# Kernel tuning notes

Measured on AMD Instinct MI355X. Metric: run time of the kernel, lower is better.

Reference implementation:

```python
import jax, jax.numpy as jnp
import numpy as np

HEADS = 16
DIM_HEAD = 64
SCALE = DIM_HEAD ** -0.5
NEG = -jnp.finfo(jnp.float32).max


def setup_inputs() -> dict:
    key = jax.random.key(0)
    ks = jax.random.split(key, 5)
    b, n, dim = 2, 2048, 1024
    inner = HEADS * DIM_HEAD
    s = dim ** -0.5  # keep pre-softmax logits well-scaled
    return {
        "x": jax.random.normal(ks[0], (b, n, dim), jnp.float32),
        "mask": jnp.ones((b, n), dtype=bool),
        "Wq": jax.random.normal(ks[1], (dim, inner), jnp.float32) * s,
        "Wk": jax.random.normal(ks[2], (dim, inner), jnp.float32) * s,
        "Wv": jax.random.normal(ks[3], (dim, inner), jnp.float32) * s,
        "Wo": jax.random.normal(ks[4], (inner, dim), jnp.float32) * s,
    }


def reference(x, mask, Wq, Wk, Wv, Wo):
    b, n, _ = x.shape
    # projections, split heads: b n (h d) -> b h n d
    def split(t):
        return t.reshape(b, n, HEADS, DIM_HEAD).transpose(0, 2, 1, 3)
    q = split(x @ Wq)
    k = split(x @ Wk)
    v = split(x @ Wv)
    dots = jnp.einsum("bhid,bhjd->bhij", q, k) * SCALE  # [b,h,n,n]
    # padding mask: b j -> b 1 1 j
    dots = jnp.where(mask[:, None, None, :], dots, NEG)
    # causal mask (strict upper triangle masked)
    causal = jnp.triu(jnp.ones((n, n), dtype=bool), k=1)
    dots = jnp.where(causal, NEG, dots)
    attn = jax.nn.softmax(dots, axis=-1)
    out = jnp.einsum("bhij,bhjd->bhid", attn, v)
    out = out.transpose(0, 2, 1, 3).reshape(b, n, HEADS * DIM_HEAD)
    return out @ Wo
```

## Files before the change

kernel.cpp:

```cpp
#include <hip/hip_runtime.h>
#include <hip/hip_bf16.h>

typedef __bf16 bf16x8 __attribute__((ext_vector_type(8)));
typedef float f32x4 __attribute__((ext_vector_type(4)));
typedef unsigned short u16;
typedef unsigned int u32;

#define MFMA16(A, B, C) __builtin_amdgcn_mfma_f32_16x16x32_bf16((A), (B), (C), 0, 0, 0)

#define BATCH 2
#define SEQ   2048
#define DIM   1024
#define NHEAD 16
#define DHEAD 64
#define MROWS 4096
#define Q_SCALE 0.18033688f

__device__ __forceinline__ u16 f2bf(float f) {
    unsigned int u = __float_as_uint(f);
    u += 0x7fff + ((u >> 16) & 1);
    return (u16)(u >> 16);
}

__device__ __forceinline__ u32 pk2bf(float a, float b) {
    __hip_bfloat162 c = __float22bfloat162_rn(float2{a, b});
    u32 r;
    __builtin_memcpy(&r, &c, 4);
    return r;
}

__device__ __forceinline__ void glds16(const u16* g, u16* l) {
    __builtin_amdgcn_global_load_lds(
        (const __attribute__((address_space(1))) u32*)g,
        (__attribute__((address_space(3))) u32*)l, 16, 0, 0);
}

__global__ __launch_bounds__(256) void cvt_x(const float* __restrict__ x,
                                             u16* __restrict__ xb) {
    int i = (blockIdx.x * 256 + threadIdx.x) * 8;
    float4 a = *(const float4*)(x + i);
    float4 b = *(const float4*)(x + i + 4);
    u16 o[8] = {f2bf(a.x), f2bf(a.y), f2bf(a.z), f2bf(a.w),
                f2bf(b.x), f2bf(b.y), f2bf(b.z), f2bf(b.w)};
    *(uint4*)(xb + i) = *(uint4*)o;
}

__global__ __launch_bounds__(256) void cvt_w_t(const float* __restrict__ wq,
                                               const float* __restrict__ wk,
                                               const float* __restrict__ wv,
                                               const float* __restrict__ wo,
                                               u16* __restrict__ wt) {
    __shared__ u16 tile[64][65];
    const float* W = (blockIdx.z == 0) ? wq : (blockIdx.z == 1) ? wk
                   : (blockIdx.z == 2) ? wv : wo;
    u16* out = wt + (size_t)blockIdx.z * DIM * DIM;
    int k0 = blockIdx.x * 64;
    int n0 = blockIdx.y * 64;
    int t = threadIdx.x;
    int c = t & 63, r4 = t >> 6;
#pragma unroll
    for (int i = 0; i < 16; i++) {
        int row = i * 4 + r4;
        tile[row][c] = f2bf(W[(size_t)(k0 + row) * DIM + n0 + c]);
    }
    __syncthreads();
#pragma unroll
    for (int i = 0; i < 16; i++) {
        int row = i * 4 + r4;
        out[(size_t)(n0 + row) * DIM + k0 + c] = tile[c][row];
    }
}

__global__ __launch_bounds__(256) void gemm_qkv(const u16* __restrict__ xb,
                                                const u16* __restrict__ wt,
                                                u16* __restrict__ qb,
                                                u16* __restrict__ kb,
                                                u16* __restrict__ vtb) {
    __shared__ __align__(16) u16 As[128 * 32];
    __shared__ __align__(16) u16 Bs[128 * 32];
    const int z = blockIdx.z;
    const u16* W = wt + (size_t)z * DIM * DIM;
    const int m0 = blockIdx.y * 128, n0 = blockIdx.x * 128;
    const int t = threadIdx.x, w = t >> 6, lane = t & 63;
    const int quad = lane >> 4, l16 = lane & 15;
    const int wm = (w >> 1) * 64, wn = (w & 1) * 64;
    const int srow = lane >> 2, skc = (lane & 3) * 8;

    f32x4 acc[4][4] = {};
    for (int k0 = 0; k0 < DIM; k0 += 32) {
        if (k0) __syncthreads();
#pragma unroll
        for (int j = 0; j < 2; j++) {
            int rb = w * 32 + j * 16;
            glds16(&xb[(size_t)(m0 + rb + srow) * DIM + k0 + skc], &As[rb * 32]);
            glds16(&W[(size_t)(n0 + rb + srow) * DIM + k0 + skc], &Bs[rb * 32]);
        }
        __syncthreads();

        bf16x8 af[4], bfr[4];
#pragma unroll
        for (int mt = 0; mt < 4; mt++)
            af[mt] = *(const bf16x8*)&As[(wm + mt * 16 + l16) * 32 + quad * 8];
#pragma unroll
        for (int nt = 0; nt < 4; nt++)
            bfr[nt] = *(const bf16x8*)&Bs[(wn + nt * 16 + l16) * 32 + quad * 8];
#pragma unroll
        for (int mt = 0; mt < 4; mt++)
#pragma unroll
            for (int nt = 0; nt < 4; nt++)
                acc[mt][nt] = MFMA16(af[mt], bfr[nt], acc[mt][nt]);
    }
    const float sc = (z == 0) ? Q_SCALE : 1.0f;
#pragma unroll
    for (int mt = 0; mt < 4; mt++)
#pragma unroll
        for (int nt = 0; nt < 4; nt++)
#pragma unroll
            for (int r = 0; r < 4; r++) {
                int gm = m0 + wm + mt * 16 + quad * 4 + r;
                int gc = n0 + wn + nt * 16 + l16;
                int bi = gm >> 11, si = gm & (SEQ - 1);
                int h = gc >> 6, d = gc & 63;
                u16 v = f2bf(acc[mt][nt][r] * sc);
                if (z == 0)
                    qb[(((size_t)bi * NHEAD + h) * SEQ + si) * DHEAD + d] = v;
                else if (z == 1)
                    kb[(((size_t)bi * NHEAD + h) * SEQ + si) * DHEAD + d] = v;
                else
                    vtb[(((size_t)bi * NHEAD + h) * DHEAD + d) * SEQ + si] = v;
            }
}

#define LPAD 72
__global__ __launch_bounds__(256) void attn(const u16* __restrict__ qg,
                                            const u16* __restrict__ kg,
                                            const u16* __restrict__ vtg,
                                            u16* __restrict__ og) {
    __shared__ __align__(16) u16 Ks[2][64 * LPAD];
    __shared__ __align__(16) u16 Vs[2][64 * LPAD];
    __shared__ __align__(16) u16 Ps[64 * LPAD];

    const int bh = blockIdx.y;
    const int t = threadIdx.x, w = t >> 6, lane = t & 63;
    const int quad = lane >> 4, l16 = lane & 15;
    const int srow = t >> 2, sc16 = (t & 3) * 16;
    const size_t qkrow = (size_t)bh * SEQ;
    const size_t vrow = (size_t)bh * DHEAD;
    const int bi = bh >> 4, h = bh & 15;

    uint4 pk0, pk1, pv0, pv1;
    auto prefetch = [&](int j0) {
        const u16* kp = &kg[(qkrow + j0 + srow) * DHEAD + sc16];
        pk0 = *(const uint4*)kp;
        pk1 = *(const uint4*)(kp + 8);
        const u16* vp = &vtg[(vrow + srow) * SEQ + j0 + sc16];
        pv0 = *(const uint4*)vp;
        pv1 = *(const uint4*)(vp + 8);
    };

    u16* prow = &Ps[(w * 16 + l16) * LPAD];

    for (int half = 0; half < 2; half++) {
        const int qt = half ? (31 - (int)blockIdx.x) : (int)blockIdx.x;
        const int q0 = qt * 64;
        const int last = qt;
        const int rowmin = q0 + w * 16;
        const int rowq = rowmin + l16;

        const u16* qp = qg + (qkrow + rowq) * DHEAD;
        bf16x8 aq0 = *(const bf16x8*)(qp + quad * 8);
        bf16x8 aq1 = *(const bf16x8*)(qp + 32 + quad * 8);

        f32x4 accO[4] = {};
        float l_part = 0.f;

        prefetch(0);
        __syncthreads();

        for (int jt = 0; jt <= last; jt++) {
            const int buf = jt & 1;
            u16* ksb = &Ks[buf][0];
            u16* vsb = &Vs[buf][0];
            *(uint4*)&ksb[srow * LPAD + sc16] = pk0;
            *(uint4*)&ksb[srow * LPAD + sc16 + 8] = pk1;
            *(uint4*)&vsb[srow * LPAD + sc16] = pv0;
            *(uint4*)&vsb[srow * LPAD + sc16 + 8] = pv1;
            __syncthreads();
            if (jt < last) prefetch((jt + 1) * 64);

            const int j0 = jt * 64;
            if (j0 > rowmin + 15) continue;
            const bool need_mask = (j0 + 63 > rowmin);

            f32x4 s[4];
#pragma unroll
            for (int nt = 0; nt < 4; nt++) {
                bf16x8 ak0 = *(const bf16x8*)&ksb[(nt * 16 + l16) * LPAD + quad * 8];
                bf16x8 ak1 = *(const bf16x8*)&ksb[(nt * 16 + l16) * LPAD + 32 + quad * 8];
                f32x4 a = {};
                a = MFMA16(ak0, aq0, a);
                a = MFMA16(ak1, aq1, a);
                s[nt] = a;
            }

#pragma unroll
            for (int nt = 0; nt < 4; nt++) {
                float p[4];
                if (need_mask) {
                    int kbase = j0 + nt * 16 + quad * 4;
#pragma unroll
                    for (int r = 0; r < 4; r++)
                        p[r] = (kbase + r > rowq) ? 0.f
                             : __builtin_amdgcn_exp2f(s[nt][r]);
                } else {
#pragma unroll
                    for (int r = 0; r < 4; r++)
                        p[r] = __builtin_amdgcn_exp2f(s[nt][r]);
                }
                l_part += (p[0] + p[1]) + (p[2] + p[3]);
                uint2 pkd = {pk2bf(p[0], p[1]), pk2bf(p[2], p[3])};
                *(uint2*)&prow[nt * 16 + quad * 4] = pkd;
            }

            bf16x8 bp0 = *(const bf16x8*)&prow[quad * 8];
            bf16x8 bp1 = *(const bf16x8*)&prow[32 + quad * 8];
#pragma unroll
            for (int mt = 0; mt < 4; mt++) {
                bf16x8 av0 = *(const bf16x8*)&vsb[(mt * 16 + l16) * LPAD + quad * 8];
                bf16x8 av1 = *(const bf16x8*)&vsb[(mt * 16 + l16) * LPAD + 32 + quad * 8];
                accO[mt] = MFMA16(av0, bp0, accO[mt]);
                accO[mt] = MFMA16(av1, bp1, accO[mt]);
            }
        }

        l_part += __shfl_xor(l_part, 16);
        l_part += __shfl_xor(l_part, 32);
        float rl = 1.0f / l_part;
        size_t obase = ((size_t)bi * SEQ + rowq) * DIM + h * DHEAD;
#pragma unroll
        for (int mt = 0; mt < 4; mt++) {
            uint2 pkd = {pk2bf(accO[mt][0] * rl, accO[mt][1] * rl),
                         pk2bf(accO[mt][2] * rl, accO[mt][3] * rl)};
            *(uint2*)&og[obase + mt * 16 + quad * 4] = pkd;
        }
    }
}

__global__ __launch_bounds__(256) void gemm_out(const u16* __restrict__ ob,
                                                const u16* __restrict__ wot,
                                                float* __restrict__ out) {
    __shared__ __align__(16) u16 As[64 * 32];
    __shared__ __align__(16) u16 Bs[128 * 32];
    const int m0 = blockIdx.y * 64, n0 = blockIdx.x * 128;
    const int t = threadIdx.x, w = t >> 6, lane = t & 63;
    const int quad = lane >> 4, l16 = lane & 15;
    const int wm = (w >> 1) * 32, wn = (w & 1) * 64;
    const int srow = lane >> 2, skc = (lane & 3) * 8;

    f32x4 acc[2][4] = {};
    for (int k0 = 0; k0 < DIM; k0 += 32) {
        if (k0) __syncthreads();
        glds16(&ob[(size_t)(m0 + w * 16 + srow) * DIM + k0 + skc], &As[w * 16 * 32]);
#pragma unroll
        for (int j = 0; j < 2; j++) {
            int rb = w * 32 + j * 16;
            glds16(&wot[(size_t)(n0 + rb + srow) * DIM + k0 + skc], &Bs[rb * 32]);
        }
        __syncthreads();

        bf16x8 af[2], bfr[4];
#pragma unroll
        for (int mt = 0; mt < 2; mt++)
            af[mt] = *(const bf16x8*)&As[(wm + mt * 16 + l16) * 32 + quad * 8];
#pragma unroll
        for (int nt = 0; nt < 4; nt++)
            bfr[nt] = *(const bf16x8*)&Bs[(wn + nt * 16 + l16) * 32 + quad * 8];
#pragma unroll
        for (int mt = 0; mt < 2; mt++)
#pragma unroll
            for (int nt = 0; nt < 4; nt++)
                acc[mt][nt] = MFMA16(af[mt], bfr[nt], acc[mt][nt]);
    }
#pragma unroll
    for (int mt = 0; mt < 2; mt++)
#pragma unroll
        for (int nt = 0; nt < 4; nt++)
#pragma unroll
            for (int r = 0; r < 4; r++) {
                int gm = m0 + wm + mt * 16 + quad * 4 + r;
                int gc = n0 + wn + nt * 16 + l16;
                out[(size_t)gm * DIM + gc] = acc[mt][nt][r];
            }
}

extern "C" void kernel_launch(void* const* d_in, const int* in_sizes, int n_in,
                              void* d_out, int out_size, void* d_ws, size_t ws_size,
                              hipStream_t stream) {
    const float* x  = (const float*)d_in[0];
    const float* wq = (const float*)d_in[2];
    const float* wk = (const float*)d_in[3];
    const float* wv = (const float*)d_in[4];
    const float* wo = (const float*)d_in[5];
    float* out = (float*)d_out;

    char* ws = (char*)d_ws;
    u16* xb  = (u16*)(ws);
    u16* wt  = (u16*)(ws + (8ull  << 20));
    u16* qb  = (u16*)(ws + (16ull << 20));
    u16* kb  = (u16*)(ws + (24ull << 20));
    u16* vtb = (u16*)(ws + (32ull << 20));
    u16* obf = (u16*)(ws + (40ull << 20));

    cvt_x<<<MROWS * DIM / (256 * 8), 256, 0, stream>>>(x, xb);
    cvt_w_t<<<dim3(16, 16, 4), 256, 0, stream>>>(wq, wk, wv, wo, wt);
    gemm_qkv<<<dim3(DIM / 128, MROWS / 128, 3), 256, 0, stream>>>(xb, wt, qb, kb, vtb);
    attn<<<dim3(16, BATCH * NHEAD), 256, 0, stream>>>(qb, kb, vtb, obf);
    gemm_out<<<dim3(DIM / 128, MROWS / 64), 256, 0, stream>>>(
        obf, wt + 3ull * DIM * DIM, out);
}
```

Measured before the change: 191.7 us.

## Rework attention kernel to 32x32 MFMA with key-split waves and async LDS staging

Replaces the attention inner loop's 16x16x32 MFMAs with 32x32x16 MFMAs. Each wave now owns 32 query rows and one 32-key half of each 64-key tile, and the two key halves are reduced through shared memory at the end. K/V tiles are staged with direct global-to-LDS loads (glds16) into XOR-swizzled unpadded buffers, issued before compute to overlap with the current tile. This aims to cut LDS fragment loads and register-staging overhead, at the cost of extra shared memory for the output reduction, an additional barrier, and waves idling on masked key halves.

```diff
diff --git a/kernel.cpp b/kernel.cpp
--- a/kernel.cpp
+++ b/kernel.cpp
@@ -3,10 +3,12 @@
 
 typedef __bf16 bf16x8 __attribute__((ext_vector_type(8)));
 typedef float f32x4 __attribute__((ext_vector_type(4)));
+typedef float f32x16 __attribute__((ext_vector_type(16)));
 typedef unsigned short u16;
 typedef unsigned int u32;
 
 #define MFMA16(A, B, C) __builtin_amdgcn_mfma_f32_16x16x32_bf16((A), (B), (C), 0, 0, 0)
+#define MFMA32(A, B, C) __builtin_amdgcn_mfma_f32_32x32x16_bf16((A), (B), (C), 0, 0, 0)
 
 #define BATCH 2
 #define SEQ   2048
@@ -136,112 +138,131 @@
                                             const u16* __restrict__ kg,
                                             const u16* __restrict__ vtg,
                                             u16* __restrict__ og) {
-    __shared__ __align__(16) u16 Ks[2][64 * LPAD];
-    __shared__ __align__(16) u16 Vs[2][64 * LPAD];
+    __shared__ __align__(16) u16 Ks[2][64 * 64];
+    __shared__ __align__(16) u16 Vs[2][64 * 64];
     __shared__ __align__(16) u16 Ps[64 * LPAD];
+    __shared__ __align__(16) float Os[4096];
+    __shared__ float Ls[64];
 
     const int bh = blockIdx.y;
     const int t = threadIdx.x, w = t >> 6, lane = t & 63;
-    const int quad = lane >> 4, l16 = lane & 15;
-    const int srow = t >> 2, sc16 = (t & 3) * 16;
-    const size_t qkrow = (size_t)bh * SEQ;
-    const size_t vrow = (size_t)bh * DHEAD;
-    const int bi = bh >> 4, h = bh & 15;
-
-    uint4 pk0, pk1, pv0, pv1;
-    auto prefetch = [&](int j0) {
-        const u16* kp = &kg[(qkrow + j0 + srow) * DHEAD + sc16];
-        pk0 = *(const uint4*)kp;
-        pk1 = *(const uint4*)(kp + 8);
-        const u16* vp = &vtg[(vrow + srow) * SEQ + j0 + sc16];
-        pv0 = *(const uint4*)vp;
-        pv1 = *(const uint4*)(vp + 8);
+    const int l31 = lane & 31, hf = lane >> 5;
+    const int wq = w >> 1, kh = w & 1;
+    const int lrow = lane >> 3, lx = lane & 7;
+    const size_t qkbase = (size_t)bh * SEQ;
+    const size_t vbase = (size_t)bh * DHEAD;
+    const int bi = bh >> 4, hh = bh & 15;
+    float4* Osf4 = (float4*)Os;
+
+    auto stage = [&](int j0, int buf) {
+#pragma unroll
+        for (int g = 0; g < 2; g++) {
+            int R = w * 16 + g * 8;
+            int m = R + lrow;
+            int c = lx ^ (m & 7);
+            glds16(&kg[(qkbase + j0 + m) * DHEAD + c * 8], &Ks[buf][R * 64]);
+            glds16(&vtg[(vbase + m) * SEQ + j0 + c * 8], &Vs[buf][R * 64]);
+        }
     };
-
-    u16* prow = &Ps[(w * 16 + l16) * LPAD];
 
     for (int half = 0; half < 2; half++) {
         const int qt = half ? (31 - (int)blockIdx.x) : (int)blockIdx.x;
         const int q0 = qt * 64;
         const int last = qt;
-        const int rowmin = q0 + w * 16;
-        const int rowq = rowmin + l16;
-
-        const u16* qp = qg + (qkrow + rowq) * DHEAD;
-        bf16x8 aq0 = *(const bf16x8*)(qp + quad * 8);
-        bf16x8 aq1 = *(const bf16x8*)(qp + 32 + quad * 8);
-
-        f32x4 accO[4] = {};
+        const int rowmin = q0 + wq * 32;
+        const int qrow = rowmin + l31;
+
+        bf16x8 bq[4];
+#pragma unroll
+        for (int s = 0; s < 4; s++)
+            bq[s] = *(const bf16x8*)&qg[(qkbase + qrow) * DHEAD + s * 16 + hf * 8];
+
+        f32x16 accO[2] = {};
         float l_part = 0.f;
 
-        prefetch(0);
+        stage(0, 0);
         __syncthreads();
 
         for (int jt = 0; jt <= last; jt++) {
             const int buf = jt & 1;
-            u16* ksb = &Ks[buf][0];
-            u16* vsb = &Vs[buf][0];
-            *(uint4*)&ksb[srow * LPAD + sc16] = pk0;
-            *(uint4*)&ksb[srow * LPAD + sc16 + 8] = pk1;
-            *(uint4*)&vsb[srow * LPAD + sc16] = pv0;
-            *(uint4*)&vsb[srow * LPAD + sc16 + 8] = pv1;
+            if (jt < last) stage((jt + 1) * 64, buf ^ 1);
+            const int j0 = jt * 64;
+
+            if (j0 + kh * 32 <= rowmin + 31) {
+                const int m = kh * 32 + l31;
+                f32x16 sa = {};
+#pragma unroll
+                for (int s = 0; s < 4; s++) {
+                    int c = 2 * s + hf;
+                    bf16x8 ak = *(const bf16x8*)
+                        &Ks[buf][(m * 8 + (c ^ (m & 7))) * 8];
+                    sa = MFMA32(ak, bq[s], sa);
+                }
+
+                const bool need_mask = (j0 + kh * 32 + 31 > rowmin);
+                u16* prow = &Ps[(wq * 32 + l31) * LPAD + kh * 32];
+#pragma unroll
+                for (int j = 0; j < 4; j++) {
+                    float p[4];
+                    int kb = j0 + kh * 32 + 8 * j + 4 * hf;
+#pragma unroll
+                    for (int i = 0; i < 4; i++) {
+                        float pv = __builtin_amdgcn_exp2f(sa[4 * j + i]);
+                        if (need_mask && (kb + i > qrow)) pv = 0.f;
+                        p[i] = pv;
+                    }
+                    l_part += (p[0] + p[1]) + (p[2] + p[3]);
+                    uint2 pkd = {pk2bf(p[0], p[1]), pk2bf(p[2], p[3])};
+                    *(uint2*)&prow[8 * j + 4 * hf] = pkd;
+                }
+
+                bf16x8 bp[2];
+#pragma unroll
+                for (int s2 = 0; s2 < 2; s2++)
+                    bp[s2] = *(const bf16x8*)&Ps[(wq * 32 + l31) * LPAD +
+                                                 kh * 32 + s2 * 16 + hf * 8];
+#pragma unroll
+                for (int mt = 0; mt < 2; mt++) {
+                    int md = mt * 32 + l31;
+#pragma unroll
+                    for (int s2 = 0; s2 < 2; s2++) {
+                        int cv = kh * 4 + s2 * 2 + hf;
+                        bf16x8 av = *(const bf16x8*)
+                            &Vs[buf][(md * 8 + (cv ^ (md & 7))) * 8];
+                        accO[mt] = MFMA32(av, bp[s2], accO[mt]);
+                    }
+                }
+            }
             __syncthreads();
-            if (jt < last) prefetch((jt + 1) * 64);
-
-            const int j0 = jt * 64;
-            if (j0 > rowmin + 15) continue;
-            const bool need_mask = (j0 + 63 > rowmin);
-
-            f32x4 s[4];
-#pragma unroll
-            for (int nt = 0; nt < 4; nt++) {
-                bf16x8 ak0 = *(const bf16x8*)&ksb[(nt * 16 + l16) * LPAD + quad * 8];
-                bf16x8 ak1 = *(const bf16x8*)&ksb[(nt * 16 + l16) * LPAD + 32 + quad * 8];
-                f32x4 a = {};
-                a = MFMA16(ak0, aq0, a);
-                a = MFMA16(ak1, aq1, a);
-                s[nt] = a;
-            }
-
-#pragma unroll
-            for (int nt = 0; nt < 4; nt++) {
-                float p[4];
-                if (need_mask) {
-                    int kbase = j0 + nt * 16 + quad * 4;
-#pragma unroll
-                    for (int r = 0; r < 4; r++)
-                        p[r] = (kbase + r > rowq) ? 0.f
-                             : __builtin_amdgcn_exp2f(s[nt][r]);
-                } else {
-#pragma unroll
-                    for (int r = 0; r < 4; r++)
-                        p[r] = __builtin_amdgcn_exp2f(s[nt][r]);
+        }
+
+        float l2 = l_part + __shfl_xor(l_part, 32);
+        if (kh == 1) {
+            Ls[wq * 32 + l31] = l2;
+#pragma unroll
+            for (int mt = 0; mt < 2; mt++)
+#pragma unroll
+                for (int j = 0; j < 4; j++)
+                    Osf4[((wq * 2 + mt) * 8 + 2 * j + hf) * 32 + l31] =
+                        float4{accO[mt][4 * j], accO[mt][4 * j + 1],
+                               accO[mt][4 * j + 2], accO[mt][4 * j + 3]};
+        }
+        __syncthreads();
+        if (kh == 0) {
+            float rl = 1.0f / (l2 + Ls[wq * 32 + l31]);
+            size_t obase = ((size_t)bi * SEQ + qrow) * DIM + hh * DHEAD;
+#pragma unroll
+            for (int mt = 0; mt < 2; mt++)
+#pragma unroll
+                for (int j = 0; j < 4; j++) {
+                    float4 o = Osf4[((wq * 2 + mt) * 8 + 2 * j + hf) * 32 + l31];
+                    float v0 = (accO[mt][4 * j]     + o.x) * rl;
+                    float v1 = (accO[mt][4 * j + 1] + o.y) * rl;
+                    float v2 = (accO[mt][4 * j + 2] + o.z) * rl;
+                    float v3 = (accO[mt][4 * j + 3] + o.w) * rl;
+                    uint2 pkd = {pk2bf(v0, v1), pk2bf(v2, v3)};
+                    *(uint2*)&og[obase + mt * 32 + 8 * j + 4 * hf] = pkd;
                 }
-                l_part += (p[0] + p[1]) + (p[2] + p[3]);
-                uint2 pkd = {pk2bf(p[0], p[1]), pk2bf(p[2], p[3])};
-                *(uint2*)&prow[nt * 16 + quad * 4] = pkd;
-            }
-
-            bf16x8 bp0 = *(const bf16x8*)&prow[quad * 8];
-            bf16x8 bp1 = *(const bf16x8*)&prow[32 + quad * 8];
-#pragma unroll
-            for (int mt = 0; mt < 4; mt++) {
-                bf16x8 av0 = *(const bf16x8*)&vsb[(mt * 16 + l16) * LPAD + quad * 8];
-                bf16x8 av1 = *(const bf16x8*)&vsb[(mt * 16 + l16) * LPAD + 32 + quad * 8];
-                accO[mt] = MFMA16(av0, bp0, accO[mt]);
-                accO[mt] = MFMA16(av1, bp1, accO[mt]);
-            }
-        }
-
-        l_part += __shfl_xor(l_part, 16);
-        l_part += __shfl_xor(l_part, 32);
-        float rl = 1.0f / l_part;
-        size_t obase = ((size_t)bi * SEQ + rowq) * DIM + h * DHEAD;
-#pragma unroll
-        for (int mt = 0; mt < 4; mt++) {
-            uint2 pkd = {pk2bf(accO[mt][0] * rl, accO[mt][1] * rl),
-                         pk2bf(accO[mt][2] * rl, accO[mt][3] * rl)};
-            *(uint2*)&og[obase + mt * 16 + quad * 4] = pkd;
         }
     }
 }
```

Result: slower. 197.5 us (+3.0%).

## Split attention key tile across warp pairs with 32-row query tiles

Applied to the files above, without the earlier changes.

Changes the attention warp decomposition so each warp handles 32 query rows and half of the 64-key tile, instead of 16 query rows over all 64 keys. K and V fragments loaded from shared memory are reused across two query subtiles, which raises MFMA work per LDS load. The two key-half partial outputs and row sums are combined through a new fp32 shared buffer and a barrier at the end of each query tile. This costs extra shared memory, which may lower occupancy, plus the merge step and more accumulator registers.

```diff
diff --git a/kernel.cpp b/kernel.cpp
--- a/kernel.cpp
+++ b/kernel.cpp
@@ -132,6 +132,7 @@
 }
 
 #define LPAD 72
+#define OSTR 68
 __global__ __launch_bounds__(256) void attn(const u16* __restrict__ qg,
                                             const u16* __restrict__ kg,
                                             const u16* __restrict__ vtg,
@@ -139,40 +140,44 @@
     __shared__ __align__(16) u16 Ks[2][64 * LPAD];
     __shared__ __align__(16) u16 Vs[2][64 * LPAD];
     __shared__ __align__(16) u16 Ps[64 * LPAD];
+    __shared__ __align__(16) float Os[64 * OSTR];
+    __shared__ float Ls[64];
 
     const int bh = blockIdx.y;
     const int t = threadIdx.x, w = t >> 6, lane = t & 63;
     const int quad = lane >> 4, l16 = lane & 15;
+    const int wq32 = (w >> 1) * 32, kh = w & 1, kh32 = kh * 32;
     const int srow = t >> 2, sc16 = (t & 3) * 16;
-    const size_t qkrow = (size_t)bh * SEQ;
-    const size_t vrow = (size_t)bh * DHEAD;
-    const int bi = bh >> 4, h = bh & 15;
+    const size_t qkbase = (size_t)bh * SEQ;
+    const size_t vbase = (size_t)bh * DHEAD;
+    const int bi = bh >> 4, hh = bh & 15;
 
     uint4 pk0, pk1, pv0, pv1;
     auto prefetch = [&](int j0) {
-        const u16* kp = &kg[(qkrow + j0 + srow) * DHEAD + sc16];
+        const u16* kp = &kg[(qkbase + j0 + srow) * DHEAD + sc16];
         pk0 = *(const uint4*)kp;
         pk1 = *(const uint4*)(kp + 8);
-        const u16* vp = &vtg[(vrow + srow) * SEQ + j0 + sc16];
+        const u16* vp = &vtg[(vbase + srow) * SEQ + j0 + sc16];
         pv0 = *(const uint4*)vp;
         pv1 = *(const uint4*)(vp + 8);
     };
-
-    u16* prow = &Ps[(w * 16 + l16) * LPAD];
 
     for (int half = 0; half < 2; half++) {
         const int qt = half ? (31 - (int)blockIdx.x) : (int)blockIdx.x;
         const int q0 = qt * 64;
         const int last = qt;
-        const int rowmin = q0 + w * 16;
-        const int rowq = rowmin + l16;
-
-        const u16* qp = qg + (qkrow + rowq) * DHEAD;
-        bf16x8 aq0 = *(const bf16x8*)(qp + quad * 8);
-        bf16x8 aq1 = *(const bf16x8*)(qp + 32 + quad * 8);
-
-        f32x4 accO[4] = {};
-        float l_part = 0.f;
+        const int rowmin = q0 + wq32;
+
+        bf16x8 bq[2][2];
+#pragma unroll
+        for (int ct = 0; ct < 2; ct++) {
+            const u16* qp = qg + (qkbase + q0 + wq32 + ct * 16 + l16) * DHEAD;
+            bq[ct][0] = *(const bf16x8*)(qp + quad * 8);
+            bq[ct][1] = *(const bf16x8*)(qp + 32 + quad * 8);
+        }
+
+        f32x4 accO[4][2] = {};
+        float l_part[2] = {0.f, 0.f};
 
         prefetch(0);
         __syncthreads();
@@ -189,59 +194,117 @@
             if (jt < last) prefetch((jt + 1) * 64);
 
             const int j0 = jt * 64;
-            if (j0 > rowmin + 15) continue;
-            const bool need_mask = (j0 + 63 > rowmin);
-
-            f32x4 s[4];
-#pragma unroll
-            for (int nt = 0; nt < 4; nt++) {
-                bf16x8 ak0 = *(const bf16x8*)&ksb[(nt * 16 + l16) * LPAD + quad * 8];
-                bf16x8 ak1 = *(const bf16x8*)&ksb[(nt * 16 + l16) * LPAD + 32 + quad * 8];
-                f32x4 a = {};
-                a = MFMA16(ak0, aq0, a);
-                a = MFMA16(ak1, aq1, a);
-                s[nt] = a;
-            }
-
-#pragma unroll
-            for (int nt = 0; nt < 4; nt++) {
-                float p[4];
-                if (need_mask) {
-                    int kbase = j0 + nt * 16 + quad * 4;
-#pragma unroll
-                    for (int r = 0; r < 4; r++)
-                        p[r] = (kbase + r > rowq) ? 0.f
-                             : __builtin_amdgcn_exp2f(s[nt][r]);
-                } else {
-#pragma unroll
-                    for (int r = 0; r < 4; r++)
-                        p[r] = __builtin_amdgcn_exp2f(s[nt][r]);
+            if (j0 + kh32 > rowmin + 31) continue;
+            const bool need_mask = (j0 + kh32 + 31 > rowmin);
+
+            bf16x8 ak[2][2];
+#pragma unroll
+            for (int nt = 0; nt < 2; nt++) {
+                const u16* kr = &ksb[(kh32 + nt * 16 + l16) * LPAD];
+                ak[nt][0] = *(const bf16x8*)(kr + quad * 8);
+                ak[nt][1] = *(const bf16x8*)(kr + 32 + quad * 8);
+            }
+            f32x4 s[2][2];
+#pragma unroll
+            for (int nt = 0; nt < 2; nt++)
+#pragma unroll
+                for (int ct = 0; ct < 2; ct++) {
+                    f32x4 a = {};
+                    a = MFMA16(ak[nt][0], bq[ct][0], a);
+                    a = MFMA16(ak[nt][1], bq[ct][1], a);
+                    s[nt][ct] = a;
                 }
-                l_part += (p[0] + p[1]) + (p[2] + p[3]);
-                uint2 pkd = {pk2bf(p[0], p[1]), pk2bf(p[2], p[3])};
-                *(uint2*)&prow[nt * 16 + quad * 4] = pkd;
-            }
-
-            bf16x8 bp0 = *(const bf16x8*)&prow[quad * 8];
-            bf16x8 bp1 = *(const bf16x8*)&prow[32 + quad * 8];
+
+            if (need_mask) {
+#pragma unroll
+                for (int ct = 0; ct < 2; ct++) {
+                    int qv = q0 + wq32 + ct * 16 + l16;
+#pragma unroll
+                    for (int nt = 0; nt < 2; nt++) {
+                        int kb = j0 + kh32 + nt * 16 + quad * 4;
+                        float p[4];
+#pragma unroll
+                        for (int r = 0; r < 4; r++)
+                            p[r] = (kb + r > qv) ? 0.f
+                                 : __builtin_amdgcn_exp2f(s[nt][ct][r]);
+                        l_part[ct] += (p[0] + p[1]) + (p[2] + p[3]);
+                        uint2 pkd = {pk2bf(p[0], p[1]), pk2bf(p[2], p[3])};
+                        *(uint2*)&Ps[(wq32 + ct * 16 + l16) * LPAD + kh32 +
+                                     nt * 16 + quad * 4] = pkd;
+                    }
+                }
+            } else {
+#pragma unroll
+                for (int ct = 0; ct < 2; ct++)
+#pragma unroll
+                    for (int nt = 0; nt < 2; nt++) {
+                        float p[4];
+#pragma unroll
+                        for (int r = 0; r < 4; r++)
+                            p[r] = __builtin_amdgcn_exp2f(s[nt][ct][r]);
+                        l_part[ct] += (p[0] + p[1]) + (p[2] + p[3]);
+                        uint2 pkd = {pk2bf(p[0], p[1]), pk2bf(p[2], p[3])};
+                        *(uint2*)&Ps[(wq32 + ct * 16 + l16) * LPAD + kh32 +
+                                     nt * 16 + quad * 4] = pkd;
+                    }
+            }
+
+            bf16x8 bp[2];
+#pragma unroll
+            for (int ct = 0; ct < 2; ct++)
+                bp[ct] = *(const bf16x8*)&Ps[(wq32 + ct * 16 + l16) * LPAD +
+                                             kh32 + quad * 8];
 #pragma unroll
             for (int mt = 0; mt < 4; mt++) {
-                bf16x8 av0 = *(const bf16x8*)&vsb[(mt * 16 + l16) * LPAD + quad * 8];
-                bf16x8 av1 = *(const bf16x8*)&vsb[(mt * 16 + l16) * LPAD + 32 + quad * 8];
-                accO[mt] = MFMA16(av0, bp0, accO[mt]);
-                accO[mt] = MFMA16(av1, bp1, accO[mt]);
-            }
-        }
-
-        l_part += __shfl_xor(l_part, 16);
-        l_part += __shfl_xor(l_part, 32);
-        float rl = 1.0f / l_part;
-        size_t obase = ((size_t)bi * SEQ + rowq) * DIM + h * DHEAD;
-#pragma unroll
-        for (int mt = 0; mt < 4; mt++) {
-            uint2 pkd = {pk2bf(accO[mt][0] * rl, accO[mt][1] * rl),
-                         pk2bf(accO[mt][2] * rl, accO[mt][3] * rl)};
-            *(uint2*)&og[obase + mt * 16 + quad * 4] = pkd;
+                bf16x8 av = *(const bf16x8*)&vsb[(mt * 16 + l16) * LPAD +
+                                                 kh32 + quad * 8];
+#pragma unroll
+                for (int ct = 0; ct < 2; ct++)
+                    accO[mt][ct] = MFMA16(av, bp[ct], accO[mt][ct]);
+            }
+        }
+
+        float l2[2];
+#pragma unroll
+        for (int ct = 0; ct < 2; ct++) {
+            float l = l_part[ct];
+            l += __shfl_xor(l, 16);
+            l += __shfl_xor(l, 32);
+            l2[ct] = l;
+        }
+        if (kh == 1) {
+            if (quad == 0) {
+                Ls[wq32 + l16] = l2[0];
+                Ls[wq32 + 16 + l16] = l2[1];
+            }
+#pragma unroll
+            for (int mt = 0; mt < 4; mt++)
+#pragma unroll
+                for (int ct = 0; ct < 2; ct++)
+                    *(float4*)&Os[(wq32 + ct * 16 + l16) * OSTR + mt * 16 +
+                                  quad * 4] =
+                        float4{accO[mt][ct][0], accO[mt][ct][1],
+                               accO[mt][ct][2], accO[mt][ct][3]};
+        }
+        __syncthreads();
+        if (kh == 0) {
+#pragma unroll
+            for (int ct = 0; ct < 2; ct++) {
+                int q = q0 + wq32 + ct * 16 + l16;
+                float rl = 1.0f / (l2[ct] + Ls[wq32 + ct * 16 + l16]);
+                size_t obase = ((size_t)bi * SEQ + q) * DIM + hh * DHEAD;
+#pragma unroll
+                for (int mt = 0; mt < 4; mt++) {
+                    float4 o = *(float4*)&Os[(wq32 + ct * 16 + l16) * OSTR +
+                                             mt * 16 + quad * 4];
+                    float v0 = (accO[mt][ct][0] + o.x) * rl;
+                    float v1 = (accO[mt][ct][1] + o.y) * rl;
+                    float v2 = (accO[mt][ct][2] + o.z) * rl;
+                    float v3 = (accO[mt][ct][3] + o.w) * rl;
+                    uint2 pkd = {pk2bf(v0, v1), pk2bf(v2, v3)};
+                    *(uint2*)&og[obase + mt * 16 + quad * 4] = pkd;
+                }
+            }
         }
     }
 }
```

New measurement: 187.1 us. 2.4% less time.
